# Kernel tuning notes

Hardware: AMD Instinct MI355X
Metric: run time of the kernel (lower is better)

The kernel has to match this reference:

```python
import jax, jax.numpy as jnp
import numpy as np

N, E, F, H, G, C = 50000, 800000, 768, 256, 512, 2  # H = nhid*2 (nhid=128), G graphs, C classes
NHID = 128


def setup_inputs() -> dict:
    key = jax.random.key(0)
    ks = jax.random.split(key, 18)
    s = 0.05
    x = jax.random.normal(ks[0], (N, F), jnp.float32)
    edge_index = jax.random.randint(ks[1], (2, E), 0, N, dtype=jnp.int32)
    # sorted batch vector; every graph non-empty so the 'first node per graph' gather is valid
    batch = ((jnp.arange(N) * G) // N).astype(jnp.int32)
    return {
        "x": x,
        "edge_index": edge_index,
        "batch": batch,
        # GATConv 1 (in=F, out=H, heads=1)
        "W1": jax.random.normal(ks[2], (F, H), jnp.float32) * s,
        "as1": jax.random.normal(ks[3], (H,), jnp.float32) * s,
        "ad1": jax.random.normal(ks[4], (H,), jnp.float32) * s,
        "b1": jnp.zeros((H,), jnp.float32),
        # GATConv 2 (in=H, out=H)
        "W2": jax.random.normal(ks[5], (H, H), jnp.float32) * s,
        "as2": jax.random.normal(ks[6], (H,), jnp.float32) * s,
        "ad2": jax.random.normal(ks[7], (H,), jnp.float32) * s,
        "b2": jnp.zeros((H,), jnp.float32),
        # fc0: num_features -> nhid (news branch)
        "W0": jax.random.normal(ks[8], (F, NHID), jnp.float32) * s,
        "b0": jnp.zeros((NHID,), jnp.float32),
        # fc1: 2*nhid -> nhid (used twice, as in the source)
        "Wf1": jax.random.normal(ks[9], (H, NHID), jnp.float32) * s,
        "bf1": jnp.zeros((NHID,), jnp.float32),
        # fc2: nhid -> num_classes
        "Wf2": jax.random.normal(ks[10], (NHID, C), jnp.float32) * s,
        "bf2": jnp.zeros((C,), jnp.float32),
    }


def _gat(x, src, dst, W, a_s, a_d, b):
    # PyG GATConv, heads=1, concat=True, negative_slope=0.2, self-loops pre-appended to src/dst.
    h = x @ W                                   # [N, H]
    e = jax.nn.leaky_relu((h @ a_s)[src] + (h @ a_d)[dst], 0.2)  # [E+N]
    m = jax.ops.segment_max(e, dst, num_segments=N)
    ex = jnp.exp(e - m[dst])                    # stable segment softmax numerator
    denom = jax.ops.segment_sum(ex, dst, num_segments=N)
    agg = jax.ops.segment_sum(ex[:, None] * h[src], dst, num_segments=N)  # [N, H]
    return agg / denom[:, None] + b


def reference(x, edge_index, batch, W1, as1, ad1, b1, W2, as2, ad2, b2, W0, b0, Wf1, bf1, Wf2, bf2):
    loop = jnp.arange(N, dtype=edge_index.dtype)
    src = jnp.concatenate([edge_index[0], loop])  # add self-loops (PyG default)
    dst = jnp.concatenate([edge_index[1], loop])
    h = jax.nn.selu(_gat(x, src, dst, W1, as1, ad1, b1))
    h = jax.nn.selu(_gat(h, src, dst, W2, as2, ad2, b2))
    # global mean pool over graphs
    cnt = jax.ops.segment_sum(jnp.ones((N,), h.dtype), batch, num_segments=G)
    pooled = jax.nn.selu(jax.ops.segment_sum(h, batch, num_segments=G) / cnt[:, None])
    z = jax.nn.selu(pooled @ Wf1 + bf1)
    # dropout(p=0.5) in eval mode -> identity
    # concat branch: first node of each graph (news root)
    first_idx = jax.ops.segment_min(jnp.arange(N), batch, num_segments=G)
    news = jax.nn.relu(x[first_idx] @ W0 + b0)
    z = jnp.concatenate([z, news], axis=1)       # [G, 2*nhid]
    z = jax.nn.relu(z @ Wf1 + bf1)
    return jax.nn.log_softmax(z @ Wf2 + bf2, axis=-1)
```

## Files before the change

kernel.cpp:

```cpp
#include <hip/hip_runtime.h>
#include <hip/hip_bf16.h>
#include <cstdint>
#include <cstddef>

#define NN 50000
#define EE 800000
#define FF 768
#define HH 256
#define GG 512
#define CC 2
#define NHIDD 128
#define ETOT (EE + NN)
#define NCHUNK 49

typedef __attribute__((ext_vector_type(8))) short bf16x8;
typedef __attribute__((ext_vector_type(4))) float f32x4;
typedef __attribute__((ext_vector_type(8))) unsigned short us8;

__device__ __forceinline__ float b2f(unsigned short u){
  union { float f; uint32_t i; } v; v.i = ((uint32_t)u) << 16; return v.f;
}
__device__ __forceinline__ unsigned short f2b(float f){
  uint32_t u = __float_as_uint(f);
  uint32_t r = (u + 0x7fffu + ((u >> 16) & 1u)) >> 16;
  return (unsigned short)r;
}
__device__ __forceinline__ float selu_f(float x){
  const float lam = 1.0507009873554805f, alp = 1.6732632423543772f;
  return x > 0.f ? lam * x : lam * alp * (__expf(x) - 1.f);
}

__global__ __launch_bounds__(256) void swizzleW(const float* __restrict__ W,
                                                unsigned short* __restrict__ Wsw, int K){
  int i = blockIdx.x * 256 + threadIdx.x;
  if (i < K * HH){
    int k = i / HH, n = i % HH;
    Wsw[(size_t)(k >> 5) * 8192 + n * 32 + (k & 31)] = f2b(W[i]);
  }
}

__global__ __launch_bounds__(256) void zero_deg(int* deg){
  int i = blockIdx.x * 256 + threadIdx.x;
  if (i < NN) deg[i] = 0;
}

__global__ __launch_bounds__(256) void deg_kernel(const int* __restrict__ dstA, int* __restrict__ deg){
  int i = blockIdx.x * 256 + threadIdx.x;
  if (i < ETOT){
    int d = (i < EE) ? dstA[i] : (i - EE);
    atomicAdd(&deg[d], 1);
  }
}

__global__ __launch_bounds__(256) void scanA(const int* __restrict__ deg, int* __restrict__ bsum){
  __shared__ int red[256];
  int c = blockIdx.x, tid = threadIdx.x;
  int base = c * 1024 + tid * 4;
  int s = 0;
#pragma unroll
  for (int j = 0; j < 4; j++){ int idx = base + j; if (idx < NN) s += deg[idx]; }
  red[tid] = s; __syncthreads();
  for (int off = 128; off > 0; off >>= 1){
    if (tid < off) red[tid] += red[tid + off];
    __syncthreads();
  }
  if (tid == 0) bsum[c] = red[0];
}

__global__ void scanB(int* bsum){
  if (threadIdx.x == 0){
    int run = 0;
    for (int i = 0; i < NCHUNK; i++){ int v = bsum[i]; bsum[i] = run; run += v; }
  }
}

__global__ __launch_bounds__(256) void scanC(const int* __restrict__ deg, const int* __restrict__ bsum,
                                             int* __restrict__ row_ptr, int* __restrict__ fill_ptr){
  __shared__ int ts[256];
  int c = blockIdx.x, tid = threadIdx.x;
  int base = c * 1024 + tid * 4;
  int v[4]; int s = 0;
#pragma unroll
  for (int j = 0; j < 4; j++){ int idx = base + j; v[j] = (idx < NN) ? deg[idx] : 0; s += v[j]; }
  ts[tid] = s; __syncthreads();
  for (int off = 1; off < 256; off <<= 1){
    int add = (tid >= off) ? ts[tid - off] : 0;
    __syncthreads();
    ts[tid] += add;
    __syncthreads();
  }
  int run = ts[tid] - s + bsum[c];
#pragma unroll
  for (int j = 0; j < 4; j++){
    int idx = base + j;
    if (idx < NN){ row_ptr[idx] = run; fill_ptr[idx] = run; }
    run += v[j];
  }
  if (c == 0 && tid == 0) row_ptr[NN] = ETOT;
}

__global__ __launch_bounds__(256) void fill_kernel(const int* __restrict__ srcA, const int* __restrict__ dstA,
                                                   int* __restrict__ fill_ptr, int* __restrict__ csr_src){
  int i = blockIdx.x * 256 + threadIdx.x;
  if (i < ETOT){
    int s = (i < EE) ? srcA[i] : (i - EE);
    int d = (i < EE) ? dstA[i] : (i - EE);
    int pos = atomicAdd(&fill_ptr[d], 1);
    csr_src[pos] = s;
  }
}

template<int K, bool AF32>
__global__ __launch_bounds__(256) void gemm_mfma(const void* __restrict__ Ap,
                                                 const unsigned short* __restrict__ Wsw,
                                                 unsigned short* __restrict__ out, int M){
  __shared__ unsigned short Al[2][32][72];
  const int tid = threadIdx.x;
  const int m0 = blockIdx.x * 32;
  const int lane = tid & 63, w = tid >> 6;
  const int koff = (lane >> 4) * 8;
  const int arow = lane & 15;
  const int nrow = w * 64 + (lane & 15);
  const int srow = tid >> 3, skc = (tid & 7) * 8;
  const bool rowok = (m0 + srow < M);

  f32x4 acc[2][4];
#pragma unroll
  for (int rt = 0; rt < 2; rt++)
#pragma unroll
    for (int ct = 0; ct < 4; ct++) acc[rt][ct] = (f32x4){0.f, 0.f, 0.f, 0.f};

  auto stageA = [&](int ks, int buf){
    if (rowok){
      if (AF32){
        const float* Af = (const float*)Ap;
        size_t ab = (size_t)(m0 + srow) * K + ks * 64 + skc;
        float4 f0 = *(const float4*)&Af[ab];
        float4 f1 = *(const float4*)&Af[ab + 4];
        us8 v;
        v[0] = f2b(f0.x); v[1] = f2b(f0.y); v[2] = f2b(f0.z); v[3] = f2b(f0.w);
        v[4] = f2b(f1.x); v[5] = f2b(f1.y); v[6] = f2b(f1.z); v[7] = f2b(f1.w);
        *(us8*)&Al[buf][srow][skc] = v;
      } else {
        const unsigned short* Au = (const unsigned short*)Ap;
        *(us8*)&Al[buf][srow][skc] = *(const us8*)&Au[(size_t)(m0 + srow) * K + ks * 64 + skc];
      }
    } else {
      us8 z = {0,0,0,0,0,0,0,0}; *(us8*)&Al[buf][srow][skc] = z;
    }
  };

  constexpr int NIT = K / 64;
  stageA(0, 0);
  bf16x8 bcur[2][4];
#pragma unroll
  for (int k2 = 0; k2 < 2; k2++){
    const unsigned short* bp = Wsw + ((size_t)k2 * 8192 + (size_t)nrow * 32 + koff);
#pragma unroll
    for (int ct = 0; ct < 4; ct++) bcur[k2][ct] = *(const bf16x8*)(bp + ct * 512);
  }
  __syncthreads();

  for (int ks = 0; ks < NIT; ks++){
    bf16x8 bnext[2][4];
    if (ks + 1 < NIT){
#pragma unroll
      for (int k2 = 0; k2 < 2; k2++){
        const unsigned short* bp = Wsw + ((size_t)((ks + 1) * 2 + k2) * 8192 + (size_t)nrow * 32 + koff);
#pragma unroll
        for (int ct = 0; ct < 4; ct++) bnext[k2][ct] = *(const bf16x8*)(bp + ct * 512);
      }
      stageA(ks + 1, (ks + 1) & 1);
    }
    bf16x8 af[2][2];
#pragma unroll
    for (int k2 = 0; k2 < 2; k2++)
#pragma unroll
      for (int rt = 0; rt < 2; rt++)
        af[k2][rt] = *(const bf16x8*)&Al[ks & 1][rt * 16 + arow][k2 * 32 + koff];
#pragma unroll
    for (int k2 = 0; k2 < 2; k2++)
#pragma unroll
      for (int rt = 0; rt < 2; rt++)
#pragma unroll
        for (int ct = 0; ct < 4; ct++)
          acc[rt][ct] = __builtin_amdgcn_mfma_f32_16x16x32_bf16(af[k2][rt], bcur[k2][ct], acc[rt][ct], 0, 0, 0);
    if (ks + 1 < NIT){
#pragma unroll
      for (int k2 = 0; k2 < 2; k2++)
#pragma unroll
        for (int ct = 0; ct < 4; ct++) bcur[k2][ct] = bnext[k2][ct];
    }
    __syncthreads();
  }

#pragma unroll
  for (int rt = 0; rt < 2; rt++){
    int mbase = m0 + rt * 16 + (lane >> 4) * 4;
#pragma unroll
    for (int r = 0; r < 4; r++){
      int m = mbase + r;
      if (m < M){
        size_t ro = (size_t)m * HH + w * 64 + (lane & 15);
        out[ro + 0]  = f2b(acc[rt][0][r]);
        out[ro + 16] = f2b(acc[rt][1][r]);
        out[ro + 32] = f2b(acc[rt][2][r]);
        out[ro + 48] = f2b(acc[rt][3][r]);
      }
    }
  }
}

__global__ __launch_bounds__(256) void alsald_kernel(const unsigned short* __restrict__ h,
    const float* __restrict__ a_s, const float* __restrict__ a_d,
    float* __restrict__ als, float* __restrict__ ald){
  int node = blockIdx.x * 4 + (threadIdx.x >> 6);
  int lane = threadIdx.x & 63;
  if (node >= NN) return;
  ushort4 hv = *(const ushort4*)&h[(size_t)node * HH + lane * 4];
  float4 as4 = *(const float4*)&a_s[lane * 4];
  float4 ad4 = *(const float4*)&a_d[lane * 4];
  float h0 = b2f(hv.x), h1 = b2f(hv.y), h2 = b2f(hv.z), h3 = b2f(hv.w);
  float s = h0 * as4.x + h1 * as4.y + h2 * as4.z + h3 * as4.w;
  float d = h0 * ad4.x + h1 * ad4.y + h2 * ad4.z + h3 * ad4.w;
  for (int off = 32; off > 0; off >>= 1){ s += __shfl_xor(s, off); d += __shfl_xor(d, off); }
  if (lane == 0){ als[node] = s; ald[node] = d; }
}

__global__ __launch_bounds__(256) void agg_wave(const unsigned short* __restrict__ h,
    const float* __restrict__ als, const float* __restrict__ ald,
    const int* __restrict__ row_ptr, const int* __restrict__ csr_src,
    const float* __restrict__ bias, unsigned short* __restrict__ outp){
  int node = blockIdx.x * 4 + (threadIdx.x >> 6);
  int lane = threadIdx.x & 63;
  if (node >= NN) return;
  int base = row_ptr[node];
  int deg  = row_ptr[node + 1] - base;
  float aldd = ald[node];
  float den = 0.f;
  float a0 = 0.f, a1 = 0.f, a2 = 0.f, a3 = 0.f;
  const size_t fo = (size_t)lane * 4;
  for (int p0 = 0; p0 < deg; p0 += 64){
    int cnt = min(64, deg - p0);
    float ev = 0.f; int s = 0;
    if (lane < cnt){
      s = csr_src[base + p0 + lane];
      float v = als[s] + aldd;
      v = v > 0.f ? v : 0.2f * v;
      ev = __expf(v);
    }
    den += ev;
    int j = 0;
    for (; j + 2 <= cnt; j += 2){
      float e0 = __shfl(ev, j), e1 = __shfl(ev, j + 1);
      int s0 = __shfl(s, j), s1 = __shfl(s, j + 1);
      ushort4 g0 = *(const ushort4*)&h[(size_t)s0 * HH + fo];
      ushort4 g1 = *(const ushort4*)&h[(size_t)s1 * HH + fo];
      a0 += e0 * b2f(g0.x) + e1 * b2f(g1.x);
      a1 += e0 * b2f(g0.y) + e1 * b2f(g1.y);
      a2 += e0 * b2f(g0.z) + e1 * b2f(g1.z);
      a3 += e0 * b2f(g0.w) + e1 * b2f(g1.w);
    }
    for (; j < cnt; j++){
      float e0 = __shfl(ev, j); int s0 = __shfl(s, j);
      ushort4 g0 = *(const ushort4*)&h[(size_t)s0 * HH + fo];
      a0 += e0 * b2f(g0.x); a1 += e0 * b2f(g0.y); a2 += e0 * b2f(g0.z); a3 += e0 * b2f(g0.w);
    }
  }
  for (int off = 32; off > 0; off >>= 1) den += __shfl_xor(den, off);
  float inv = 1.f / den;
  float4 b4 = *(const float4*)&bias[fo];
  ushort4 o;
  o.x = f2b(selu_f(a0 * inv + b4.x));
  o.y = f2b(selu_f(a1 * inv + b4.y));
  o.z = f2b(selu_f(a2 * inv + b4.z));
  o.w = f2b(selu_f(a3 * inv + b4.w));
  *(ushort4*)&outp[(size_t)node * HH + fo] = o;
}

__global__ __launch_bounds__(256) void first_kernel(const int* __restrict__ batch, int* __restrict__ first_idx){
  int n = blockIdx.x * 256 + threadIdx.x;
  if (n < NN){
    int b = batch[n];
    if (n == 0 || batch[n - 1] != b) first_idx[b] = n;
  }
  if (blockIdx.x == 0 && threadIdx.x == 0) first_idx[GG] = NN;
}

__global__ __launch_bounds__(256) void pool_kernel(const unsigned short* __restrict__ x3,
    const int* __restrict__ first_idx, float* __restrict__ pooled){
  int g = blockIdx.x, f = threadIdx.x;
  int s = first_idx[g], e = first_idx[g + 1];
  float acc = 0.f;
  for (int n = s; n < e; n++) acc += b2f(x3[(size_t)n * HH + f]);
  pooled[g * HH + f] = selu_f(acc / (float)(e - s));
}

__global__ __launch_bounds__(128) void z1_kernel(const float* __restrict__ pooled,
    const float* __restrict__ Wf1, const float* __restrict__ bf1,
    float* __restrict__ z1){
  __shared__ float pr[HH];
  int g = blockIdx.x, t = threadIdx.x;
  pr[t] = pooled[g * HH + t];
  pr[t + 128] = pooled[g * HH + t + 128];
  __syncthreads();
  float acc = 0.f;
  for (int k = 0; k < HH; k++) acc += pr[k] * Wf1[k * NHIDD + t];
  z1[g * NHIDD + t] = selu_f(acc + bf1[t]);
}

__global__ __launch_bounds__(128) void news_kernel(const float* __restrict__ x,
    const int* __restrict__ first_idx, const float* __restrict__ W0,
    const float* __restrict__ b0, float* __restrict__ znews){
  __shared__ float xr[FF];
  int g = blockIdx.x, t = threadIdx.x;
  int root = first_idx[g];
  for (int k = t; k < FF; k += 128) xr[k] = x[(size_t)root * FF + k];
  __syncthreads();
  float acc = 0.f;
  for (int k = 0; k < FF; k++) acc += xr[k] * W0[k * NHIDD + t];
  acc += b0[t];
  znews[g * NHIDD + t] = acc > 0.f ? acc : 0.f;
}

__global__ __launch_bounds__(128) void final_kernel(const float* __restrict__ z1,
    const float* __restrict__ znews, const float* __restrict__ Wf1,
    const float* __restrict__ bf1, const float* __restrict__ Wf2,
    const float* __restrict__ bf2, float* __restrict__ out){
  __shared__ float zc[HH];
  __shared__ float l0s[2], l1s[2];
  int g = blockIdx.x, t = threadIdx.x;
  zc[t] = z1[g * NHIDD + t];
  zc[NHIDD + t] = znews[g * NHIDD + t];
  __syncthreads();
  float acc = 0.f;
  for (int k = 0; k < HH; k++) acc += zc[k] * Wf1[k * NHIDD + t];
  float z2 = acc + bf1[t]; z2 = z2 > 0.f ? z2 : 0.f;
  float p0 = z2 * Wf2[t * CC + 0];
  float p1 = z2 * Wf2[t * CC + 1];
  for (int off = 32; off > 0; off >>= 1){ p0 += __shfl_xor(p0, off); p1 += __shfl_xor(p1, off); }
  int lane = t & 63, wid = t >> 6;
  if (lane == 0){ l0s[wid] = p0; l1s[wid] = p1; }
  __syncthreads();
  if (t == 0){
    float l0 = l0s[0] + l0s[1] + bf2[0];
    float l1 = l1s[0] + l1s[1] + bf2[1];
    float mx = fmaxf(l0, l1);
    float lse = mx + logf(__expf(l0 - mx) + __expf(l1 - mx));
    out[g * CC + 0] = l0 - lse;
    out[g * CC + 1] = l1 - lse;
  }
}

extern "C" void kernel_launch(void* const* d_in, const int* in_sizes, int n_in,
                              void* d_out, int out_size, void* d_ws, size_t ws_size,
                              hipStream_t stream){
  const float* x          = (const float*)d_in[0];
  const int* edge_index   = (const int*)d_in[1];
  const int* batch        = (const int*)d_in[2];
  const float* W1  = (const float*)d_in[3];
  const float* as1 = (const float*)d_in[4];
  const float* ad1 = (const float*)d_in[5];
  const float* b1  = (const float*)d_in[6];
  const float* W2  = (const float*)d_in[7];
  const float* as2 = (const float*)d_in[8];
  const float* ad2 = (const float*)d_in[9];
  const float* b2  = (const float*)d_in[10];
  const float* W0  = (const float*)d_in[11];
  const float* b0  = (const float*)d_in[12];
  const float* Wf1 = (const float*)d_in[13];
  const float* bf1 = (const float*)d_in[14];
  const float* Wf2 = (const float*)d_in[15];
  const float* bf2 = (const float*)d_in[16];
  float* out = (float*)d_out;

  char* w = (char*)d_ws;
  size_t off = 0;
  auto alloc = [&](size_t bytes){ size_t o = off; off += (bytes + 255) & ~(size_t)255; return o; };
  unsigned short* h    = (unsigned short*)(w + alloc((size_t)NN * HH * 2));
  unsigned short* x2   = (unsigned short*)(w + alloc((size_t)NN * HH * 2));
  unsigned short* Wsw1 = (unsigned short*)(w + alloc((size_t)FF * HH * 2));
  unsigned short* Wsw2 = (unsigned short*)(w + alloc((size_t)HH * HH * 2));
  float* als     = (float*)(w + alloc((size_t)NN * 4));
  float* ald     = (float*)(w + alloc((size_t)NN * 4));
  int*   deg     = (int*)(w + alloc((size_t)NN * 4));
  int*   row_ptr = (int*)(w + alloc((size_t)(NN + 1) * 4));
  int*   fillp   = (int*)(w + alloc((size_t)NN * 4));
  int*   csr_src = (int*)(w + alloc((size_t)ETOT * 4));
  int*   bsum    = (int*)(w + alloc(64 * 4));
  int*   firsti  = (int*)(w + alloc((size_t)(GG + 1) * 4));
  float* pooled  = (float*)(w + alloc((size_t)GG * HH * 4));
  float* z1      = (float*)(w + alloc((size_t)GG * NHIDD * 4));
  float* znews   = (float*)(w + alloc((size_t)GG * NHIDD * 4));

  const int* srcA = edge_index;
  const int* dstA = edge_index + EE;

  swizzleW<<<(FF * HH + 255) / 256, 256, 0, stream>>>(W1, Wsw1, FF);
  swizzleW<<<(HH * HH + 255) / 256, 256, 0, stream>>>(W2, Wsw2, HH);

  zero_deg<<<(NN + 255) / 256, 256, 0, stream>>>(deg);
  deg_kernel<<<(ETOT + 255) / 256, 256, 0, stream>>>(dstA, deg);
  scanA<<<NCHUNK, 256, 0, stream>>>(deg, bsum);
  scanB<<<1, 64, 0, stream>>>(bsum);
  scanC<<<NCHUNK, 256, 0, stream>>>(deg, bsum, row_ptr, fillp);
  fill_kernel<<<(ETOT + 255) / 256, 256, 0, stream>>>(srcA, dstA, fillp, csr_src);

  const int gemm_grid = (NN + 31) / 32;
  gemm_mfma<FF, true><<<gemm_grid, 256, 0, stream>>>((const void*)x, Wsw1, h, NN);
  alsald_kernel<<<(NN + 3) / 4, 256, 0, stream>>>(h, as1, ad1, als, ald);
  agg_wave<<<(NN + 3) / 4, 256, 0, stream>>>(h, als, ald, row_ptr, csr_src, b1, x2);
  gemm_mfma<HH, false><<<gemm_grid, 256, 0, stream>>>((const void*)x2, Wsw2, h, NN);
  alsald_kernel<<<(NN + 3) / 4, 256, 0, stream>>>(h, as2, ad2, als, ald);
  agg_wave<<<(NN + 3) / 4, 256, 0, stream>>>(h, als, ald, row_ptr, csr_src, b2, x2);
  first_kernel<<<(NN + 255) / 256, 256, 0, stream>>>(batch, firsti);
  pool_kernel<<<GG, 256, 0, stream>>>(x2, firsti, pooled);
  z1_kernel<<<GG, 128, 0, stream>>>(pooled, Wf1, bf1, z1);
  news_kernel<<<GG, 128, 0, stream>>>(x, firsti, W0, b0, znews);
  final_kernel<<<GG, 128, 0, stream>>>(z1, znews, Wf1, bf1, Wf2, bf2, out);
}
```

Before: 605.4 us.

## Stage full A tile into LDS upfront and drop per-iteration barriers

The GEMM now loads the entire 32xK A tile into shared memory at the start, with all loads issued together, rather than double-buffering 64-wide K slices. This removes the __syncthreads at every K step and exposes more memory-level parallelism in the A loads. The cost is more LDS per block (about 49KB for K=768), which can reduce occupancy, and no overlap between A loads and MFMA work.

```diff
diff --git a/kernel.cpp b/kernel.cpp
--- a/kernel.cpp
+++ b/kernel.cpp
@@ -114,15 +114,14 @@
 __global__ __launch_bounds__(256) void gemm_mfma(const void* __restrict__ Ap,
                                                  const unsigned short* __restrict__ Wsw,
                                                  unsigned short* __restrict__ out, int M){
-  __shared__ unsigned short Al[2][32][72];
+  constexpr int KP = K + 8;
+  __shared__ unsigned short Al[32][KP];
   const int tid = threadIdx.x;
   const int m0 = blockIdx.x * 32;
   const int lane = tid & 63, w = tid >> 6;
   const int koff = (lane >> 4) * 8;
   const int arow = lane & 15;
   const int nrow = w * 64 + (lane & 15);
-  const int srow = tid >> 3, skc = (tid & 7) * 8;
-  const bool rowok = (m0 + srow < M);
 
   f32x4 acc[2][4];
 #pragma unroll
@@ -130,54 +129,56 @@
 #pragma unroll
     for (int ct = 0; ct < 4; ct++) acc[rt][ct] = (f32x4){0.f, 0.f, 0.f, 0.f};
 
-  auto stageA = [&](int ks, int buf){
-    if (rowok){
+  constexpr int C8 = K / 8;
+  constexpr int ROUNDS = (32 * C8) / 256;
+#pragma unroll
+  for (int j = 0; j < ROUNDS; j++){
+    int q = j * 256 + tid;
+    int row = q / C8, c8 = q - row * C8;
+    int gm = m0 + row;
+    us8 v;
+    if (gm < M){
       if (AF32){
         const float* Af = (const float*)Ap;
-        size_t ab = (size_t)(m0 + srow) * K + ks * 64 + skc;
-        float4 f0 = *(const float4*)&Af[ab];
-        float4 f1 = *(const float4*)&Af[ab + 4];
-        us8 v;
+        const float4* p = (const float4*)&Af[(size_t)gm * K + c8 * 8];
+        float4 f0 = p[0], f1 = p[1];
         v[0] = f2b(f0.x); v[1] = f2b(f0.y); v[2] = f2b(f0.z); v[3] = f2b(f0.w);
         v[4] = f2b(f1.x); v[5] = f2b(f1.y); v[6] = f2b(f1.z); v[7] = f2b(f1.w);
-        *(us8*)&Al[buf][srow][skc] = v;
       } else {
-        const unsigned short* Au = (const unsigned short*)Ap;
-        *(us8*)&Al[buf][srow][skc] = *(const us8*)&Au[(size_t)(m0 + srow) * K + ks * 64 + skc];
+        v = *(const us8*)&((const unsigned short*)Ap)[(size_t)gm * K + c8 * 8];
       }
     } else {
-      us8 z = {0,0,0,0,0,0,0,0}; *(us8*)&Al[buf][srow][skc] = z;
-    }
-  };
+      v = (us8){0,0,0,0,0,0,0,0};
+    }
+    *(us8*)&Al[row][c8 * 8] = v;
+  }
+
+  const unsigned short* bbase = Wsw + ((size_t)nrow * 32 + koff);
+  bf16x8 bcur[2][4];
+#pragma unroll
+  for (int k2 = 0; k2 < 2; k2++)
+#pragma unroll
+    for (int ct = 0; ct < 4; ct++)
+      bcur[k2][ct] = *(const bf16x8*)(bbase + (size_t)k2 * 8192 + ct * 512);
+
+  __syncthreads();
 
   constexpr int NIT = K / 64;
-  stageA(0, 0);
-  bf16x8 bcur[2][4];
-#pragma unroll
-  for (int k2 = 0; k2 < 2; k2++){
-    const unsigned short* bp = Wsw + ((size_t)k2 * 8192 + (size_t)nrow * 32 + koff);
-#pragma unroll
-    for (int ct = 0; ct < 4; ct++) bcur[k2][ct] = *(const bf16x8*)(bp + ct * 512);
-  }
-  __syncthreads();
-
   for (int ks = 0; ks < NIT; ks++){
     bf16x8 bnext[2][4];
     if (ks + 1 < NIT){
 #pragma unroll
-      for (int k2 = 0; k2 < 2; k2++){
-        const unsigned short* bp = Wsw + ((size_t)((ks + 1) * 2 + k2) * 8192 + (size_t)nrow * 32 + koff);
-#pragma unroll
-        for (int ct = 0; ct < 4; ct++) bnext[k2][ct] = *(const bf16x8*)(bp + ct * 512);
-      }
-      stageA(ks + 1, (ks + 1) & 1);
+      for (int k2 = 0; k2 < 2; k2++)
+#pragma unroll
+        for (int ct = 0; ct < 4; ct++)
+          bnext[k2][ct] = *(const bf16x8*)(bbase + (size_t)((ks + 1) * 2 + k2) * 8192 + ct * 512);
     }
     bf16x8 af[2][2];
 #pragma unroll
     for (int k2 = 0; k2 < 2; k2++)
 #pragma unroll
       for (int rt = 0; rt < 2; rt++)
-        af[k2][rt] = *(const bf16x8*)&Al[ks & 1][rt * 16 + arow][k2 * 32 + koff];
+        af[k2][rt] = *(const bf16x8*)&Al[rt * 16 + arow][ks * 64 + k2 * 32 + koff];
 #pragma unroll
     for (int k2 = 0; k2 < 2; k2++)
 #pragma unroll
@@ -191,7 +192,6 @@
 #pragma unroll
         for (int ct = 0; ct < 4; ct++) bcur[k2][ct] = bnext[k2][ct];
     }
-    __syncthreads();
   }
 
 #pragma unroll
```

Result: slower. 624.7 us (+3.2%).
